# Optimization experiments

Measured on AMD Instinct MI355X. Metric: run time of the kernel, lower is better.

Reference implementation:

```python
import jax, jax.numpy as jnp
import numpy as np

N_NODES = 100000
N_EDGES = 3200000
N_FEAT = 512
N_DIMS = 256
N_CLSS = 10


def setup_inputs() -> dict:
    key = jax.random.key(0)
    ks = jax.random.split(key, 9)
    x = jax.random.normal(ks[0], (N_NODES, N_FEAT), dtype=jnp.float32)
    edge_index = jax.random.randint(ks[1], (2, N_EDGES), 0, N_NODES, dtype=jnp.int64)
    edge_weight = jax.random.uniform(ks[2], (N_EDGES,), dtype=jnp.float32)
    # GCNConv params (glorot-ish scale)
    W1 = jax.random.normal(ks[3], (N_FEAT, N_DIMS), dtype=jnp.float32) / np.sqrt(N_FEAT)
    b1 = jnp.zeros((N_DIMS,), dtype=jnp.float32)
    W2 = jax.random.normal(ks[4], (N_DIMS, N_DIMS), dtype=jnp.float32) / np.sqrt(N_DIMS)
    b2 = jnp.zeros((N_DIMS,), dtype=jnp.float32)
    Wc = jax.random.normal(ks[5], (N_DIMS, N_CLSS), dtype=jnp.float32) / np.sqrt(N_DIMS)
    bc = jnp.zeros((N_CLSS,), dtype=jnp.float32)
    return {"x": x, "edge_index": edge_index, "edge_weight": edge_weight,
            "W1": W1, "b1": b1, "W2": W2, "b2": b2, "Wc": Wc, "bc": bc}


def _gcn_norm(edge_index, edge_weight, num_nodes):
    # Add self-loops with weight 1 (PyG GCNConv default, add_self_loops=True)
    loop = jnp.arange(num_nodes, dtype=edge_index.dtype)
    row = jnp.concatenate([edge_index[0], loop])
    col = jnp.concatenate([edge_index[1], loop])
    w = jnp.concatenate([edge_weight, jnp.ones((num_nodes,), dtype=edge_weight.dtype)])
    deg = jax.ops.segment_sum(w, col, num_segments=num_nodes)
    dinv = jnp.where(deg > 0, jax.lax.rsqrt(deg), 0.0)
    norm = dinv[row] * w * dinv[col]  # D^-1/2 A D^-1/2
    return row, col, norm


def _gcn_conv(x, row, col, norm, W, b, num_nodes):
    h = x @ W                                 # [N, d_out]
    msg = norm[:, None] * h[row]              # gather + scale  [E+N, d_out]
    out = jax.ops.segment_sum(msg, col, num_segments=num_nodes)  # scatter-add
    return out + b


def reference(x, edge_index, edge_weight, W1, b1, W2, b2, Wc, bc):
    n = x.shape[0]
    row, col, norm = _gcn_norm(edge_index, edge_weight, n)
    h = _gcn_conv(x, row, col, norm, W1, b1, n)
    h = jax.nn.relu(h)  # dropout is identity in eval mode
    h = _gcn_conv(h, row, col, norm, W2, b2, n)
    h = jax.nn.relu(h)
    return h @ Wc + bc  # args.task == 0 -> linear classifier
```

## Files before the change

### kernel.cpp

```cpp
#include <hip/hip_runtime.h>


typedef __attribute__((ext_vector_type(8))) _Float16 f16x8;
typedef __attribute__((ext_vector_type(4))) float f32x4;

__global__ __launch_bounds__(256) void init_kernel(float* deg, int* cnt, int* cur, int N) {
    int i = blockIdx.x * 256 + threadIdx.x;
    if (i < N) { deg[i] = 1.0f; cnt[i] = 0; cur[i] = 0; }
}

__global__ __launch_bounds__(256) void deg_cnt_kernel(const int* __restrict__ col,
                                                      const float* __restrict__ w,
                                                      float* deg, int* cnt, int E) {
    int e = blockIdx.x * 256 + threadIdx.x;
    if (e < E) {
        int c = col[e];
        atomicAdd(&deg[c], w[e]);
        atomicAdd(&cnt[c], 1);
    }
}

__global__ __launch_bounds__(256) void dinv_kernel(float* deg, int N) {
    int i = blockIdx.x * 256 + threadIdx.x;
    if (i < N) deg[i] = rsqrtf(deg[i]);
}

__global__ __launch_bounds__(1024) void scan_kernel(const int* __restrict__ cnt,
                                                    int* __restrict__ off, int N) {
    __shared__ int sm[1024];
    int t = threadIdx.x;
    int chunk = (N + 1023) >> 10;
    int b = t * chunk;
    int e = min(b + chunk, N);
    int s = 0;
    for (int i = b; i < e; i++) s += cnt[i];
    sm[t] = s;
    __syncthreads();
#pragma unroll
    for (int d = 1; d < 1024; d <<= 1) {
        int v = (t >= d) ? sm[t - d] : 0;
        __syncthreads();
        sm[t] += v;
        __syncthreads();
    }
    int run = sm[t] - s;
    for (int i = b; i < e; i++) { off[i] = run; run += cnt[i]; }
    if (t == 1023) off[N] = sm[1023];
}

__global__ __launch_bounds__(256) void fill_kernel(const int* __restrict__ row,
                                                   const int* __restrict__ col,
                                                   const float* __restrict__ w,
                                                   const float* __restrict__ dinv,
                                                   const int* __restrict__ off, int* cur,
                                                   int* __restrict__ csr_r,
                                                   float* __restrict__ csr_n, int E) {
    int e = blockIdx.x * 256 + threadIdx.x;
    if (e >= E) return;
    int r = row[e], c = col[e];
    int pos = off[c] + atomicAdd(&cur[c], 1);
    csr_r[pos] = r;
    csr_n[pos] = dinv[r] * w[e] * dinv[c];
}

__global__ __launch_bounds__(256) void prep_b_kernel(const float* __restrict__ B,
                                                     _Float16* __restrict__ Bph,
                                                     _Float16* __restrict__ Bpl, int K) {
    int e = blockIdx.x * 256 + threadIdx.x;
    if (e >= K * 256) return;
    int k = e >> 8, n = e & 255;
    float v = B[e];
    _Float16 h = (_Float16)v;
    _Float16 lo = (_Float16)(v - (float)h);
    size_t idx = ((((size_t)(k >> 3)) * 256 + n) << 3) | (k & 7);
    Bph[idx] = h;
    Bpl[idx] = lo;
}

__global__ __launch_bounds__(256) void gemm_split_kernel(const float* __restrict__ A,
                                                         const _Float16* __restrict__ Bph,
                                                         const _Float16* __restrict__ Bpl,
                                                         float* __restrict__ C,
                                                         int M, int K) {
    int t = threadIdx.x;
    int w = t >> 6, l = t & 63;
    int lr = l & 15;
    int lg = l >> 4;
    int m0 = blockIdx.x * 64 + w * 16;

    int arow = m0 + lr;
    if (arow >= M) arow = M - 1;
    const float* Ap = A + (size_t)arow * K + lg * 8;

    f32x4 acc[16];
#pragma unroll
    for (int i = 0; i < 16; i++) acc[i] = (f32x4)0.0f;

    const f16x8* BH = (const f16x8*)Bph;
    const f16x8* BL = (const f16x8*)Bpl;

    for (int k0 = 0; k0 < K; k0 += 64) {
#pragma unroll
        for (int ks = 0; ks < 2; ks++) {
            const float* ap = Ap + k0 + ks * 32;
            f32x4 a0 = *(const f32x4*)ap;
            f32x4 a1 = *(const f32x4*)(ap + 4);
            f16x8 ah, al;
#pragma unroll
            for (int j = 0; j < 4; j++) {
                float v = a0[j];
                _Float16 hi = (_Float16)v;
                ah[j] = hi;
                al[j] = (_Float16)(v - (float)hi);
                float v2 = a1[j];
                _Float16 hi2 = (_Float16)v2;
                ah[j + 4] = hi2;
                al[j + 4] = (_Float16)(v2 - (float)hi2);
            }
            size_t bbase = ((size_t)(((k0 + ks * 32) >> 3) + lg)) * 256 + lr;
#pragma unroll
            for (int nf = 0; nf < 16; nf++) {
                f16x8 bh = BH[bbase + nf * 16];
                f16x8 bl = BL[bbase + nf * 16];
                acc[nf] = __builtin_amdgcn_mfma_f32_16x16x32_f16(ah, bh, acc[nf], 0, 0, 0);
                acc[nf] = __builtin_amdgcn_mfma_f32_16x16x32_f16(al, bh, acc[nf], 0, 0, 0);
                acc[nf] = __builtin_amdgcn_mfma_f32_16x16x32_f16(ah, bl, acc[nf], 0, 0, 0);
            }
        }
    }
#pragma unroll
    for (int nf = 0; nf < 16; nf++) {
#pragma unroll
        for (int r = 0; r < 4; r++) {
            int row = m0 + lg * 4 + r;
            if (row < M) C[(size_t)row * 256 + nf * 16 + lr] = acc[nf][r];
        }
    }
}

__global__ __launch_bounds__(256) void agg_kernel(const float* __restrict__ h,
                                                  const int* __restrict__ csr_r,
                                                  const float* __restrict__ csr_n,
                                                  const int* __restrict__ off,
                                                  const float* __restrict__ dinv,
                                                  const float* __restrict__ bias,
                                                  float* __restrict__ out, int N, int relu) {
    int lane = threadIdx.x & 63;
    int n = blockIdx.x * 4 + (threadIdx.x >> 6);
    if (n >= N) return;
    n = __builtin_amdgcn_readfirstlane(n);
    int start = off[n], end = off[n + 1];
    float d = dinv[n];
    const float4* hv = (const float4*)h;
    float4 self = hv[(size_t)n * 64 + lane];
    float sw = d * d;
    float ax = sw * self.x, ay = sw * self.y, az = sw * self.z, aw = sw * self.w;
    int j = start;
    for (; j + 4 <= end; j += 4) {
        int r0 = csr_r[j], r1 = csr_r[j + 1], r2 = csr_r[j + 2], r3 = csr_r[j + 3];
        float n0 = csr_n[j], n1 = csr_n[j + 1], n2 = csr_n[j + 2], n3 = csr_n[j + 3];
        float4 h0 = hv[(size_t)r0 * 64 + lane];
        float4 h1 = hv[(size_t)r1 * 64 + lane];
        float4 h2 = hv[(size_t)r2 * 64 + lane];
        float4 h3 = hv[(size_t)r3 * 64 + lane];
        ax += n0 * h0.x + n1 * h1.x + n2 * h2.x + n3 * h3.x;
        ay += n0 * h0.y + n1 * h1.y + n2 * h2.y + n3 * h3.y;
        az += n0 * h0.z + n1 * h1.z + n2 * h2.z + n3 * h3.z;
        aw += n0 * h0.w + n1 * h1.w + n2 * h2.w + n3 * h3.w;
    }
    for (; j < end; j++) {
        int r = csr_r[j];
        float nm = csr_n[j];
        float4 hr = hv[(size_t)r * 64 + lane];
        ax += nm * hr.x; ay += nm * hr.y; az += nm * hr.z; aw += nm * hr.w;
    }
    float4 b = ((const float4*)bias)[lane];
    ax += b.x; ay += b.y; az += b.z; aw += b.w;
    if (relu) {
        ax = fmaxf(ax, 0.f); ay = fmaxf(ay, 0.f);
        az = fmaxf(az, 0.f); aw = fmaxf(aw, 0.f);
    }
    ((float4*)out)[(size_t)n * 64 + lane] = make_float4(ax, ay, az, aw);
}

__global__ __launch_bounds__(256) void cls_kernel(const float* __restrict__ h,
                                                  const float* __restrict__ Wc,
                                                  const float* __restrict__ bc,
                                                  float* __restrict__ out, int N) {
    __shared__ float Ws[256 * 10];
    for (int i = threadIdx.x; i < 2560; i += 256) Ws[i] = Wc[i];
    __syncthreads();
    int lane = threadIdx.x & 63;
    int n = blockIdx.x * 4 + (threadIdx.x >> 6);
    if (n >= N) return;
    float4 hv4 = ((const float4*)h)[(size_t)n * 64 + lane];
    float s[10];
#pragma unroll
    for (int c = 0; c < 10; c++) {
        float v = hv4.x * Ws[(4 * lane + 0) * 10 + c] + hv4.y * Ws[(4 * lane + 1) * 10 + c] +
                  hv4.z * Ws[(4 * lane + 2) * 10 + c] + hv4.w * Ws[(4 * lane + 3) * 10 + c];
#pragma unroll
        for (int m = 32; m; m >>= 1) v += __shfl_xor(v, m, 64);
        s[c] = v;
    }
    float outv = 0.0f;
#pragma unroll
    for (int c = 0; c < 10; c++)
        if (lane == c) outv = s[c] + bc[c];
    if (lane < 10) out[(size_t)n * 10 + lane] = outv;
}

extern "C" void kernel_launch(void* const* d_in, const int* in_sizes, int n_in,
                              void* d_out, int out_size, void* d_ws, size_t ws_size,
                              hipStream_t stream) {
    const float* x  = (const float*)d_in[0];
    const int*   ei = (const int*)d_in[1];
    const float* ew = (const float*)d_in[2];
    const float* W1 = (const float*)d_in[3];
    const float* b1 = (const float*)d_in[4];
    const float* W2 = (const float*)d_in[5];
    const float* b2 = (const float*)d_in[6];
    const float* Wc = (const float*)d_in[7];
    const float* bc = (const float*)d_in[8];
    float* out = (float*)d_out;

    const int E = in_sizes[1] / 2;
    const int F = 512, D = 256;
    const int N = in_sizes[0] / F;
    const int* row = ei;
    const int* col = ei + E;

    char* ws = (char*)d_ws;
    size_t p = 0;
    auto alloc = [&](size_t bytes) -> char* {
        char* r = ws + p;
        p += (bytes + 255) & ~(size_t)255;
        return r;
    };
    float* deg   = (float*)alloc((size_t)N * 4);
    int*   off   = (int*)alloc((size_t)(N + 1) * 4);
    int*   cnt   = (int*)alloc((size_t)N * 4);
    int*   cur   = (int*)alloc((size_t)N * 4);
    int*   csr_r = (int*)alloc((size_t)E * 4);
    float* csr_n = (float*)alloc((size_t)E * 4);
    float* h     = (float*)alloc((size_t)N * D * 4);
    float* agg   = (float*)alloc((size_t)N * D * 4);
    _Float16* Bp1h = (_Float16*)alloc((size_t)F * D * 2);
    _Float16* Bp1l = (_Float16*)alloc((size_t)F * D * 2);
    _Float16* Bp2h = (_Float16*)alloc((size_t)D * D * 2);
    _Float16* Bp2l = (_Float16*)alloc((size_t)D * D * 2);
    (void)ws_size;

    init_kernel<<<(N + 255) / 256, 256, 0, stream>>>(deg, cnt, cur, N);
    deg_cnt_kernel<<<(E + 255) / 256, 256, 0, stream>>>(col, ew, deg, cnt, E);
    dinv_kernel<<<(N + 255) / 256, 256, 0, stream>>>(deg, N);
    scan_kernel<<<1, 1024, 0, stream>>>(cnt, off, N);
    fill_kernel<<<(E + 255) / 256, 256, 0, stream>>>(row, col, ew, deg, off, cur, csr_r, csr_n, E);

    prep_b_kernel<<<(F * D + 255) / 256, 256, 0, stream>>>(W1, Bp1h, Bp1l, F);
    prep_b_kernel<<<(D * D + 255) / 256, 256, 0, stream>>>(W2, Bp2h, Bp2l, D);

    int gm = (N + 63) / 64;
    gemm_split_kernel<<<gm, 256, 0, stream>>>(x, Bp1h, Bp1l, h, N, F);
    agg_kernel<<<(N + 3) / 4, 256, 0, stream>>>(h, csr_r, csr_n, off, deg, b1, agg, N, 1);
    gemm_split_kernel<<<gm, 256, 0, stream>>>(agg, Bp2h, Bp2l, h, N, D);
    agg_kernel<<<(N + 3) / 4, 256, 0, stream>>>(h, csr_r, csr_n, off, deg, b2, agg, N, 1);
    cls_kernel<<<(N + 3) / 4, 256, 0, stream>>>(agg, Wc, bc, out, N);
}
```

Baseline: 2.381 ms.

## Stage split-fp16 B tiles in shared memory and double rows per wave in GEMM

The split-precision GEMM now loads each 32-wide K slice of the hi/lo B matrices cooperatively into LDS once per block, instead of every wave reading B from global memory. Each wave now computes 32 rows (two 16-row MFMA tiles), so every B fragment is reused across both tiles and the block covers 128 rows. The aim is to cut global/L2 traffic for B and raise MFMA work per load. In exchange it doubles accumulator registers (32 f32x4 per lane), which can lower occupancy, and it adds two __syncthreads per K step with no double buffering.

```diff
diff --git a/kernel.cpp b/kernel.cpp
--- a/kernel.cpp
+++ b/kernel.cpp
@@ -82,58 +82,80 @@
                                                          const _Float16* __restrict__ Bpl,
                                                          float* __restrict__ C,
                                                          int M, int K) {
+    __shared__ f16x8 sB[2][1024];
     int t = threadIdx.x;
     int w = t >> 6, l = t & 63;
     int lr = l & 15;
     int lg = l >> 4;
-    int m0 = blockIdx.x * 64 + w * 16;
-
-    int arow = m0 + lr;
-    if (arow >= M) arow = M - 1;
-    const float* Ap = A + (size_t)arow * K + lg * 8;
-
-    f32x4 acc[16];
-#pragma unroll
-    for (int i = 0; i < 16; i++) acc[i] = (f32x4)0.0f;
-
-    const f16x8* BH = (const f16x8*)Bph;
-    const f16x8* BL = (const f16x8*)Bpl;
-
-    for (int k0 = 0; k0 < K; k0 += 64) {
-#pragma unroll
-        for (int ks = 0; ks < 2; ks++) {
-            const float* ap = Ap + k0 + ks * 32;
-            f32x4 a0 = *(const f32x4*)ap;
-            f32x4 a1 = *(const f32x4*)(ap + 4);
-            f16x8 ah, al;
+    int m0 = blockIdx.x * 128 + w * 32;
+
+    int ar0 = m0 + lr;       if (ar0 >= M) ar0 = M - 1;
+    int ar1 = m0 + 16 + lr;  if (ar1 >= M) ar1 = M - 1;
+    const float* Ap0 = A + (size_t)ar0 * K + lg * 8;
+    const float* Ap1 = A + (size_t)ar1 * K + lg * 8;
+
+    f32x4 acc0[16], acc1[16];
+#pragma unroll
+    for (int i = 0; i < 16; i++) { acc0[i] = (f32x4)0.0f; acc1[i] = (f32x4)0.0f; }
+
+    const f16x8* GHbase = (const f16x8*)Bph;
+    const f16x8* GLbase = (const f16x8*)Bpl;
+
+    for (int k0 = 0; k0 < K; k0 += 32) {
+        const f16x8* GH = GHbase + ((size_t)(k0 >> 3)) * 256;
+        const f16x8* GL = GLbase + ((size_t)(k0 >> 3)) * 256;
+        __syncthreads();
+#pragma unroll
+        for (int u = 0; u < 4; u++) {
+            int idx = u * 256 + t;
+            sB[0][idx] = GH[idx];
+            sB[1][idx] = GL[idx];
+        }
+        __syncthreads();
+
+        f16x8 ah0, al0, ah1, al1;
+        {
+            f32x4 a0 = *(const f32x4*)(Ap0 + k0);
+            f32x4 a1 = *(const f32x4*)(Ap0 + k0 + 4);
 #pragma unroll
             for (int j = 0; j < 4; j++) {
-                float v = a0[j];
-                _Float16 hi = (_Float16)v;
-                ah[j] = hi;
-                al[j] = (_Float16)(v - (float)hi);
-                float v2 = a1[j];
-                _Float16 hi2 = (_Float16)v2;
-                ah[j + 4] = hi2;
-                al[j + 4] = (_Float16)(v2 - (float)hi2);
+                float v = a0[j]; _Float16 hi = (_Float16)v;
+                ah0[j] = hi; al0[j] = (_Float16)(v - (float)hi);
+                float v2 = a1[j]; _Float16 hi2 = (_Float16)v2;
+                ah0[j + 4] = hi2; al0[j + 4] = (_Float16)(v2 - (float)hi2);
             }
-            size_t bbase = ((size_t)(((k0 + ks * 32) >> 3) + lg)) * 256 + lr;
-#pragma unroll
-            for (int nf = 0; nf < 16; nf++) {
-                f16x8 bh = BH[bbase + nf * 16];
-                f16x8 bl = BL[bbase + nf * 16];
-                acc[nf] = __builtin_amdgcn_mfma_f32_16x16x32_f16(ah, bh, acc[nf], 0, 0, 0);
-                acc[nf] = __builtin_amdgcn_mfma_f32_16x16x32_f16(al, bh, acc[nf], 0, 0, 0);
-                acc[nf] = __builtin_amdgcn_mfma_f32_16x16x32_f16(ah, bl, acc[nf], 0, 0, 0);
+            f32x4 b0 = *(const f32x4*)(Ap1 + k0);
+            f32x4 b1 = *(const f32x4*)(Ap1 + k0 + 4);
+#pragma unroll
+            for (int j = 0; j < 4; j++) {
+                float v = b0[j]; _Float16 hi = (_Float16)v;
+                ah1[j] = hi; al1[j] = (_Float16)(v - (float)hi);
+                float v2 = b1[j]; _Float16 hi2 = (_Float16)v2;
+                ah1[j + 4] = hi2; al1[j + 4] = (_Float16)(v2 - (float)hi2);
             }
         }
-    }
+
+#pragma unroll
+        for (int nf = 0; nf < 16; nf++) {
+            f16x8 bh = sB[0][lg * 256 + nf * 16 + lr];
+            f16x8 bl = sB[1][lg * 256 + nf * 16 + lr];
+            acc0[nf] = __builtin_amdgcn_mfma_f32_16x16x32_f16(ah0, bh, acc0[nf], 0, 0, 0);
+            acc0[nf] = __builtin_amdgcn_mfma_f32_16x16x32_f16(al0, bh, acc0[nf], 0, 0, 0);
+            acc0[nf] = __builtin_amdgcn_mfma_f32_16x16x32_f16(ah0, bl, acc0[nf], 0, 0, 0);
+            acc1[nf] = __builtin_amdgcn_mfma_f32_16x16x32_f16(ah1, bh, acc1[nf], 0, 0, 0);
+            acc1[nf] = __builtin_amdgcn_mfma_f32_16x16x32_f16(al1, bh, acc1[nf], 0, 0, 0);
+            acc1[nf] = __builtin_amdgcn_mfma_f32_16x16x32_f16(ah1, bl, acc1[nf], 0, 0, 0);
+        }
+    }
+
 #pragma unroll
     for (int nf = 0; nf < 16; nf++) {
 #pragma unroll
         for (int r = 0; r < 4; r++) {
-            int row = m0 + lg * 4 + r;
-            if (row < M) C[(size_t)row * 256 + nf * 16 + lr] = acc[nf][r];
+            int row0 = m0 + lg * 4 + r;
+            if (row0 < M) C[(size_t)row0 * 256 + nf * 16 + lr] = acc0[nf][r];
+            int row1 = m0 + 16 + lg * 4 + r;
+            if (row1 < M) C[(size_t)row1 * 256 + nf * 16 + lr] = acc1[nf][r];
         }
     }
 }
@@ -260,7 +282,7 @@
     prep_b_kernel<<<(F * D + 255) / 256, 256, 0, stream>>>(W1, Bp1h, Bp1l, F);
     prep_b_kernel<<<(D * D + 255) / 256, 256, 0, stream>>>(W2, Bp2h, Bp2l, D);
 
-    int gm = (N + 63) / 64;
+    int gm = (N + 127) / 128;
     gemm_split_kernel<<<gm, 256, 0, stream>>>(x, Bp1h, Bp1l, h, N, F);
     agg_kernel<<<(N + 3) / 4, 256, 0, stream>>>(h, csr_r, csr_n, off, deg, b1, agg, N, 1);
     gemm_split_kernel<<<gm, 256, 0, stream>>>(agg, Bp2h, Bp2l, h, N, D);
```

Result: faster. 2.185 ms (-8.2%).
